# Performance work log

Measured on AMD Instinct MI355X. Metric: run time of the kernel, lower is better.

## Reference

```python
import jax, jax.numpy as jnp
import numpy as np

QN, QP = -8, 7  # signed 4-bit


def round_pass(x):
    # straight-through round (forward: round-half-even like torch.round)
    return x + jax.lax.stop_gradient(jnp.round(x) - x)


def setup_inputs() -> dict:
    key = jax.random.key(0)
    ks = jax.random.split(key, 9)
    B, S, D, H = 16, 1024, 768, 3072
    def unif(k, shape):
        return jax.random.uniform(k, shape, jnp.float32, 0.02, 0.1)
    return {
        "x0": jax.random.normal(ks[0], (B, S, D), jnp.float32),
        "w1": jax.random.normal(ks[1], (H, D), jnp.float32) * 0.02,
        "b1": jax.random.normal(ks[2], (H,), jnp.float32) * 0.02,
        "alpha_w1": unif(ks[3], (H,)),
        "alpha_a1": unif(ks[4], (D,)),
        "w2": jax.random.normal(ks[5], (D, H), jnp.float32) * 0.02,
        "b2": jax.random.normal(ks[6], (D,), jnp.float32) * 0.02,
        "alpha_w2": unif(ks[7], (D,)),
        "alpha_a2": unif(ks[8], (H,)),
    }


def _quant_act(x, alpha_a):
    # ActQ_v2: per-tensor (mean of kernel-wise alpha), signed int4
    a = alpha_a.mean()
    return round_pass(jnp.clip(x / a, QN, QP))


def _quant_w(w, alpha_w):
    # LinearQ_v2: per-output-channel alpha, shape [out, in]
    return round_pass(jnp.clip(w / alpha_w[:, None], QN, QP))


def reference(x0, w1, b1, alpha_w1, alpha_a1, w2, b2, alpha_w2, alpha_a2):
    # fc1: int4 act quant, int4 weight quant, integer matmul, dequant scale + bias
    xq = _quant_act(x0, alpha_a1)                       # [B,S,D] integer-valued
    wq1 = _quant_w(w1, alpha_w1)                        # [H,D] integer-valued
    x1 = jnp.einsum('bsd,hd->bsh', xq, wq1)             # int matmul (float carrier)
    x1 = x1 * alpha_w1 * alpha_a1.mean() + b1           # per-channel dequant + bias
    x1 = jax.nn.gelu(x1, approximate=False)             # nn.GELU (exact erf)
    x1 = jnp.clip(x1, -10.0, 10.0)
    # dropout p=0.0 -> identity
    # fc2
    hq = _quant_act(x1, alpha_a2)                       # [B,S,H]
    wq2 = _quant_w(w2, alpha_w2)                        # [D,H]
    x2 = jnp.einsum('bsh,dh->bsd', hq, wq2)
    x2 = x2 * alpha_w2 * alpha_a2.mean() + b2
    return x2
```

## Files before the change

### kernel.cpp

```cpp
#include <hip/hip_runtime.h>
#include <hip/hip_bf16.h>
#include <math.h>


typedef __attribute__((ext_vector_type(4))) int i32x4;

__device__ __forceinline__ void gload_lds16(const void* g, void* l) {
  __builtin_amdgcn_global_load_lds(
      (const __attribute__((address_space(1))) void*)g,
      (__attribute__((address_space(3))) void*)l, 16, 0, 0);
}

__device__ __forceinline__ int q4_i8(float x, float a) {
  float t = x / a;
  t = fminf(fmaxf(t, -8.0f), 7.0f);
  t = rintf(t);
  return (int)t;
}

__global__ void means_k(const float* __restrict__ v1, int n1,
                        const float* __restrict__ v2, int n2,
                        float* __restrict__ out) {
  const float* src = blockIdx.x ? v2 : v1;
  const int n = blockIdx.x ? n2 : n1;
  __shared__ double red[256];
  double s = 0.0;
  for (int i = threadIdx.x; i < n; i += 256) s += (double)src[i];
  red[threadIdx.x] = s;
  __syncthreads();
  for (int st = 128; st > 0; st >>= 1) {
    if (threadIdx.x < st) red[threadIdx.x] += red[threadIdx.x + st];
    __syncthreads();
  }
  if (threadIdx.x == 0) {
    float m = (float)(red[0] / (double)n);
    out[blockIdx.x] = m;
    if (blockIdx.x == 1) {
      out[2] = 1.0f / m;
      out[3] = 0.5f * (1.0f / m);
    }
  }
}

__global__ void quant_x_k(const float* __restrict__ x,
                          unsigned* __restrict__ xq,
                          const float* __restrict__ means, int n4) {
  int i = blockIdx.x * blockDim.x + threadIdx.x;
  if (i >= n4) return;
  const float a = means[0];
  float4 v = ((const float4*)x)[i];
  unsigned u = (q4_i8(v.x, a) & 0xFF) | ((q4_i8(v.y, a) & 0xFF) << 8) |
               ((q4_i8(v.z, a) & 0xFF) << 16) | ((q4_i8(v.w, a) & 0xFF) << 24);
  xq[i] = u;
}

__global__ void quant_w_k(const float* __restrict__ w,
                          const float* __restrict__ alpha,
                          unsigned* __restrict__ wq, int C, int n4) {
  int i = blockIdx.x * blockDim.x + threadIdx.x;
  if (i >= n4) return;
  int row = (i * 4) / C;
  const float a = alpha[row];
  float4 v = ((const float4*)w)[i];
  unsigned u = (q4_i8(v.x, a) & 0xFF) | ((q4_i8(v.y, a) & 0xFF) << 8) |
               ((q4_i8(v.z, a) & 0xFF) << 16) | ((q4_i8(v.w, a) & 0xFF) << 24);
  wq[i] = u;
}

__global__ __launch_bounds__(256, 4) void gemm1_k(
    const signed char* __restrict__ A, const signed char* __restrict__ B,
    const float* __restrict__ alphaw, const float* __restrict__ bias,
    const float* __restrict__ means, signed char* __restrict__ out_b, int N,
    int K) {
  __shared__ __align__(16) signed char sA[128 * 128];
  __shared__ __align__(16) signed char sB[128 * 128];
  const int tid = threadIdx.x;
  const int w = tid >> 6;
  const int l = tid & 63;
  const int wm = w >> 1, wn = w & 1;
  const long bm0 = (long)blockIdx.y * 128;
  const long bn0 = (long)blockIdx.x * 128;

  i32x4 acc[4][4] = {};

  const int srow = l >> 3;
  const int scol = ((l & 7) * 16) ^ (srow << 4);
  const int rsw = (l & 7) << 4;

  for (int kt = 0; kt < K; kt += 128) {
    __syncthreads();
#pragma unroll
    for (int i = 0; i < 4; ++i) {
      const int c = w * 4 + i;
      const int row = c * 8 + srow;
      gload_lds16(A + (bm0 + row) * K + kt + scol, &sA[c * 1024]);
      gload_lds16(B + (bn0 + row) * K + kt + scol, &sB[c * 1024]);
    }
    __syncthreads();
#pragma unroll
    for (int kk = 0; kk < 2; ++kk) {
      const int kc = (kk * 64 + (l >> 4) * 16) ^ rsw;
      i32x4 af[4], bg[4];
#pragma unroll
      for (int m = 0; m < 4; ++m)
        af[m] = *(const i32x4*)&sA[(wm * 64 + m * 16 + (l & 15)) * 128 + kc];
#pragma unroll
      for (int n = 0; n < 4; ++n)
        bg[n] = *(const i32x4*)&sB[(wn * 64 + n * 16 + (l & 15)) * 128 + kc];
#pragma unroll
      for (int m = 0; m < 4; ++m)
#pragma unroll
        for (int n = 0; n < 4; ++n)
          acc[m][n] = __builtin_amdgcn_mfma_i32_16x16x64_i8(af[m], bg[n],
                                                            acc[m][n], 0, 0, 0);
    }
  }

  const float a1 = means[0];
  const float half_inv_a2 = means[3];

  float awa1[4], bsc[4];
  const int cc0 = (int)bn0 + wn * 64 + (l & 15);
#pragma unroll
  for (int n = 0; n < 4; ++n) {
    awa1[n] = alphaw[cc0 + n * 16] * a1;
    bsc[n] = bias[cc0 + n * 16];
  }

  const int r0 = (int)bm0 + wm * 64 + (l >> 4) * 4;

#pragma unroll
  for (int m = 0; m < 4; ++m) {
#pragma unroll
    for (int rg = 0; rg < 4; ++rg) {
      const int r = r0 + m * 16 + rg;
      signed char* prow = out_b + (size_t)r * N + cc0;
#pragma unroll
      for (int n = 0; n < 4; ++n) {
        const float f = (float)acc[m][n][rg];
        const float t = fmaf(f, awa1[n], bsc[n]);
        const float x = t * 0.70710678118654752f;
        const float az = fabsf(x);
        const float rr = __builtin_amdgcn_rcpf(fmaf(0.3275911f, az, 1.0f));
        float p = fmaf(rr, 1.061405429f, -1.453152027f);
        p = fmaf(rr, p, 1.421413741f);
        p = fmaf(rr, p, -0.284496736f);
        p = fmaf(rr, p, 0.254829592f);
        p = p * rr;
        const float e = __expf(-az * az);
        float er = fmaf(-p, e, 1.0f);
        er = copysignf(er, x);
        float qv = t * (1.0f + er) * half_inv_a2;
        qv = fminf(fmaxf(qv, -8.0f), 7.0f);
        qv = rintf(qv);
        prow[n * 16] = (signed char)(int)qv;
      }
    }
  }
}

__global__ __launch_bounds__(512, 6) void gemm2_k(
    const signed char* __restrict__ A, const signed char* __restrict__ B,
    const float* __restrict__ alphaw, const float* __restrict__ bias,
    const float* __restrict__ means, float* __restrict__ out_f, int N, int K) {
  __shared__ __align__(16) signed char sA[128 * 128];
  __shared__ __align__(16) signed char sB[128 * 128];
  const int tid = threadIdx.x;
  const int w = tid >> 6;
  const int l = tid & 63;
  const int wm = w >> 1, wn = w & 1;
  const long bm0 = (long)blockIdx.y * 128;
  const long bn0 = (long)blockIdx.x * 128;

  i32x4 acc[2][4] = {};

  const int srow = l >> 3;
  const int scol = ((l & 7) * 16) ^ (srow << 4);
  const int rsw = (l & 7) << 4;

  const signed char* gA = A + (bm0 + w * 16 + srow) * (long)K + scol;
  const signed char* gB = B + (bn0 + w * 16 + srow) * (long)K + scol;

  for (int kt = 0; kt < K; kt += 128) {
    __syncthreads();
#pragma unroll
    for (int i = 0; i < 2; ++i) {
      gload_lds16(gA + (long)i * 8 * K + kt, &sA[(w * 2 + i) * 1024]);
      gload_lds16(gB + (long)i * 8 * K + kt, &sB[(w * 2 + i) * 1024]);
    }
    __syncthreads();
#pragma unroll
    for (int kk = 0; kk < 2; ++kk) {
      const int kc = (kk * 64 + (l >> 4) * 16) ^ rsw;
      i32x4 af[2], bg[4];
#pragma unroll
      for (int m = 0; m < 2; ++m)
        af[m] = *(const i32x4*)&sA[(wm * 32 + m * 16 + (l & 15)) * 128 + kc];
#pragma unroll
      for (int n = 0; n < 4; ++n)
        bg[n] = *(const i32x4*)&sB[(wn * 64 + n * 16 + (l & 15)) * 128 + kc];
#pragma unroll
      for (int m = 0; m < 2; ++m)
#pragma unroll
        for (int n = 0; n < 4; ++n)
          acc[m][n] = __builtin_amdgcn_mfma_i32_16x16x64_i8(af[m], bg[n],
                                                            acc[m][n], 0, 0, 0);
    }
  }

  const float a2 = means[1];

  float awc[4], bsc[4];
  const int cc0 = (int)bn0 + wn * 64 + (l & 15);
#pragma unroll
  for (int n = 0; n < 4; ++n) {
    awc[n] = alphaw[cc0 + n * 16];
    bsc[n] = bias[cc0 + n * 16];
  }

  const int r0 = (int)bm0 + wm * 32 + (l >> 4) * 4;

#pragma unroll
  for (int m = 0; m < 2; ++m) {
#pragma unroll
    for (int rg = 0; rg < 4; ++rg) {
      const int r = r0 + m * 16 + rg;
      float* prow = out_f + (size_t)r * N + cc0;
#pragma unroll
      for (int n = 0; n < 4; ++n) {
        const float f = (float)acc[m][n][rg];
        float t = __fmul_rn(f, awc[n]);
        t = __fmul_rn(t, a2);
        t = __fadd_rn(t, bsc[n]);
        prow[n * 16] = t;
      }
    }
  }
}

extern "C" void kernel_launch(void* const* d_in, const int* in_sizes, int n_in,
                              void* d_out, int out_size, void* d_ws,
                              size_t ws_size, hipStream_t stream) {
  const float* x0 = (const float*)d_in[0];
  const float* w1 = (const float*)d_in[1];
  const float* b1 = (const float*)d_in[2];
  const float* aw1 = (const float*)d_in[3];
  const float* aa1 = (const float*)d_in[4];
  const float* w2 = (const float*)d_in[5];
  const float* b2 = (const float*)d_in[6];
  const float* aw2 = (const float*)d_in[7];
  const float* aa2 = (const float*)d_in[8];

  char* ws = (char*)d_ws;
  float* means = (float*)ws;
  signed char* xq = (signed char*)(ws + 256);
  signed char* wq1 = (signed char*)(ws + 12583168);
  signed char* wq2 = (signed char*)(ws + 14942464);
  signed char* hq = (signed char*)(ws + 17301760);

  means_k<<<2, 256, 0, stream>>>(aa1, 768, aa2, 3072, means);
  quant_x_k<<<12288, 256, 0, stream>>>(x0, (unsigned*)xq, means, 3145728);
  quant_w_k<<<2304, 256, 0, stream>>>(w1, aw1, (unsigned*)wq1, 768, 589824);
  quant_w_k<<<2304, 256, 0, stream>>>(w2, aw2, (unsigned*)wq2, 3072, 589824);
  dim3 g1(24, 128);
  gemm1_k<<<g1, 256, 0, stream>>>(xq, wq1, aw1, b1, means, hq, 3072, 768);
  dim3 g2(6, 128);
  gemm2_k<<<g2, 512, 0, stream>>>(hq, wq2, aw2, b2, means, (float*)d_out, 768,
                                  3072);
}
```

Baseline: 136.5 us.

## Pack GEMM1 int8 outputs into dword stores with matching permuted K layout

GEMM1's epilogue now packs the four int8 values each lane produces (columns n*16 apart) into one 32-bit store instead of four strided byte stores. This writes hq with K permuted inside each 64-column group. The w2 quantization kernel applies the same permutation to wq2, so the GEMM2 dot products stay unchanged. Launch bounds for gemm1 are raised to 5 waves per SIMD, which may limit registers. The new w2 quant kernel uses strided scalar loads instead of float4, but it is small.

```diff
diff --git a/kernel.cpp b/kernel.cpp
--- a/kernel.cpp
+++ b/kernel.cpp
@@ -67,10 +67,27 @@
   wq[i] = u;
 }
 
-__global__ __launch_bounds__(256, 4) void gemm1_k(
+__global__ void quant_w2_k(const float* __restrict__ w,
+                           const float* __restrict__ alpha,
+                           unsigned* __restrict__ wq, int nd) {
+  int i = blockIdx.x * blockDim.x + threadIdx.x;
+  if (i >= nd) return;
+  const int row = i / 768;
+  const int p = i - row * 768;
+  const int g = p >> 4, c = p & 15;
+  const float a = alpha[row];
+  const float* src = w + (size_t)row * 3072 + g * 64 + c;
+  unsigned d = 0;
+#pragma unroll
+  for (int n = 0; n < 4; ++n)
+    d |= ((unsigned)(q4_i8(src[n * 16], a) & 0xFF)) << (8 * n);
+  wq[i] = d;
+}
+
+__global__ __launch_bounds__(256, 5) void gemm1_k(
     const signed char* __restrict__ A, const signed char* __restrict__ B,
     const float* __restrict__ alphaw, const float* __restrict__ bias,
-    const float* __restrict__ means, signed char* __restrict__ out_b, int N,
+    const float* __restrict__ means, unsigned* __restrict__ out_u, int N,
     int K) {
   __shared__ __align__(16) signed char sA[128 * 128];
   __shared__ __align__(16) signed char sB[128 * 128];
@@ -128,13 +145,15 @@
   }
 
   const int r0 = (int)bm0 + wm * 64 + (l >> 4) * 4;
+  const int Nd = N >> 2;
+  const int pd = ((int)bn0 >> 2) + wn * 16 + (l & 15);
 
 #pragma unroll
   for (int m = 0; m < 4; ++m) {
 #pragma unroll
     for (int rg = 0; rg < 4; ++rg) {
       const int r = r0 + m * 16 + rg;
-      signed char* prow = out_b + (size_t)r * N + cc0;
+      unsigned d = 0;
 #pragma unroll
       for (int n = 0; n < 4; ++n) {
         const float f = (float)acc[m][n][rg];
@@ -153,8 +172,9 @@
         float qv = t * (1.0f + er) * half_inv_a2;
         qv = fminf(fmaxf(qv, -8.0f), 7.0f);
         qv = rintf(qv);
-        prow[n * 16] = (signed char)(int)qv;
+        d |= ((unsigned)((int)qv & 0xFF)) << (8 * n);
       }
+      out_u[(size_t)r * Nd + pd] = d;
     }
   }
 }
@@ -261,9 +281,10 @@
   means_k<<<2, 256, 0, stream>>>(aa1, 768, aa2, 3072, means);
   quant_x_k<<<12288, 256, 0, stream>>>(x0, (unsigned*)xq, means, 3145728);
   quant_w_k<<<2304, 256, 0, stream>>>(w1, aw1, (unsigned*)wq1, 768, 589824);
-  quant_w_k<<<2304, 256, 0, stream>>>(w2, aw2, (unsigned*)wq2, 3072, 589824);
+  quant_w2_k<<<2304, 256, 0, stream>>>(w2, aw2, (unsigned*)wq2, 589824);
   dim3 g1(24, 128);
-  gemm1_k<<<g1, 256, 0, stream>>>(xq, wq1, aw1, b1, means, hq, 3072, 768);
+  gemm1_k<<<g1, 256, 0, stream>>>(xq, wq1, aw1, b1, means, (unsigned*)hq, 3072,
+                                  768);
   dim3 g2(6, 128);
   gemm2_k<<<g2, 512, 0, stream>>>(hq, wq2, aw2, b2, means, (float*)d_out, 768,
                                   3072);
```

Result: slower. 167.8 us (+22.9%).
